# Kernel tuning notes

Hardware: AMD Instinct MI355X
Metric: run time of the kernel (lower is better)

The kernel has to match this reference:

```python
import jax, jax.numpy as jnp
import numpy as np

HEAD_SIZE = 128
B, T = 16, 2048

def setup_inputs() -> dict:
    key = jax.random.key(0)
    x = jax.random.normal(key, (B, T, 3 * HEAD_SIZE), dtype=jnp.float32)
    return {"x": x}

def reference(x) -> jnp.ndarray:
    # x: [B, T, 3*head_size] -> split into k, q, v (this order matches torch split)
    k, q, v = jnp.split(x, 3, axis=-1)  # each [B, T, D]
    d = k.shape[-1]
    scale = d ** -0.5
    # scores: [B, T, T]
    wei = jnp.einsum('bqd,bkd->bqk', q, k) * scale
    Tq = x.shape[1]
    causal = jnp.tril(jnp.ones((Tq, Tq), dtype=bool))
    wei = jnp.where(causal, wei, -jnp.inf)
    wei = jax.nn.softmax(wei, axis=-1)
    out = jnp.einsum('bqk,bkd->bqd', wei, v)  # [B, T, D]
    return out
```

## Files before the change

### kernel.cpp

```cpp
#include <hip/hip_runtime.h>

#define SEQ_T 2048
#define HDIM  128
#define NB    16
#define NTILES (SEQ_T / 64)
#define TILE_SHORTS 8192

typedef __attribute__((ext_vector_type(8))) short short8;
typedef __attribute__((ext_vector_type(4))) float float4v;
typedef __attribute__((ext_vector_type(4))) unsigned int uint4v;

#define EXP2F(x) __builtin_amdgcn_exp2f(x)

__device__ __forceinline__ unsigned int bfpack2(float a, float b) {
  unsigned int ua = __builtin_bit_cast(unsigned int, a);
  unsigned int ub = __builtin_bit_cast(unsigned int, b);
  return ((ua + 0x8000u) >> 16) | ((ub + 0x8000u) & 0xFFFF0000u);
}
__device__ __forceinline__ unsigned short f2bf(float a) {
  return (unsigned short)((__builtin_bit_cast(unsigned int, a) + 0x8000u) >> 16);
}
__device__ __forceinline__ float bf2f(unsigned short h) {
  unsigned int u = ((unsigned int)h) << 16;
  return __builtin_bit_cast(float, u);
}

__device__ __forceinline__ float dpp_max16(float x) {
  int t;
  t = __builtin_amdgcn_mov_dpp(__builtin_bit_cast(int, x), 0xB1, 0xF, 0xF, true);
  x = fmaxf(x, __builtin_bit_cast(float, t));
  t = __builtin_amdgcn_mov_dpp(__builtin_bit_cast(int, x), 0x4E, 0xF, 0xF, true);
  x = fmaxf(x, __builtin_bit_cast(float, t));
  t = __builtin_amdgcn_mov_dpp(__builtin_bit_cast(int, x), 0x141, 0xF, 0xF, true);
  x = fmaxf(x, __builtin_bit_cast(float, t));
  t = __builtin_amdgcn_mov_dpp(__builtin_bit_cast(int, x), 0x140, 0xF, 0xF, true);
  x = fmaxf(x, __builtin_bit_cast(float, t));
  return x;
}
__device__ __forceinline__ float dpp_sum16(float x) {
  int t;
  t = __builtin_amdgcn_mov_dpp(__builtin_bit_cast(int, x), 0xB1, 0xF, 0xF, true);
  x += __builtin_bit_cast(float, t);
  t = __builtin_amdgcn_mov_dpp(__builtin_bit_cast(int, x), 0x4E, 0xF, 0xF, true);
  x += __builtin_bit_cast(float, t);
  t = __builtin_amdgcn_mov_dpp(__builtin_bit_cast(int, x), 0x141, 0xF, 0xF, true);
  x += __builtin_bit_cast(float, t);
  t = __builtin_amdgcn_mov_dpp(__builtin_bit_cast(int, x), 0x140, 0xF, 0xF, true);
  x += __builtin_bit_cast(float, t);
  return x;
}

template<int CS> struct ChunkCfg;
template<> struct ChunkCfg<4> { static const int CPB = 72, SPB = 70, QB0 = 2; };
template<> struct ChunkCfg<8> { static const int CPB = 40, SPB = 36, QB0 = 4; };

__global__ __launch_bounds__(256) void prepass2(const float* __restrict__ x,
                                                unsigned short* __restrict__ kbuf,
                                                unsigned short* __restrict__ vbuf) {
  const int b = blockIdx.x >> 5;
  const int t = blockIdx.x & 31;
  const int tid = threadIdx.x;
  __shared__ __align__(16) unsigned short Klds[8192];
  __shared__ __align__(16) unsigned short Vlds[8192];

  const float* xb = x + (size_t)b * (SEQ_T * 384) + (size_t)t * 64 * 384;

  for (int i = 0; i < 8; ++i) {
    int idx = tid + i * 256;
    int row = idx >> 5, c4 = (idx & 31) << 2;
    float4v f = *(const float4v*)(xb + (size_t)row * 384 + c4);
    *(uint2*)&Klds[row * 128 + c4] = make_uint2(bfpack2(f[0], f[1]), bfpack2(f[2], f[3]));
  }
  {
    int kb = tid >> 5, db = tid & 31;
    for (int p = 0; p < 2; ++p) {
      int kbx = kb + p * 8;
      const float* vb = xb + (size_t)(4 * kbx) * 384 + 256 + 4 * db;
      float4v v0 = *(const float4v*)(vb);
      float4v v1 = *(const float4v*)(vb + 384);
      float4v v2 = *(const float4v*)(vb + 768);
      float4v v3 = *(const float4v*)(vb + 1152);
      int sl = ((kbx >> 3) << 2) | (kbx & 3);
      int o  = ((kbx >> 2) & 1) * 4;
      for (int j = 0; j < 4; ++j) {
        int d = 4 * db + j;
        *(uint2*)&Vlds[d * 64 + ((sl + d) & 7) * 8 + o] =
            make_uint2(bfpack2(v0[j], v1[j]), bfpack2(v2[j], v3[j]));
      }
    }
  }
  __syncthreads();

  unsigned short* kdst = kbuf + (size_t)blockIdx.x * TILE_SHORTS;
  unsigned short* vdst = vbuf + (size_t)blockIdx.x * TILE_SHORTS;
  for (int i = 0; i < 4; ++i) {
    int n = tid + i * 256;
    int r = n >> 4, pu = n & 15, u = (pu - r) & 15;
    *(uint4v*)&kdst[n * 8] = *(const uint4v*)&Klds[r * 128 + u * 8];
    *(uint4v*)&vdst[n * 8] = *(const uint4v*)&Vlds[n * 8];
  }
}

template<int CS>
__global__ __launch_bounds__(512, 4) void attn_chunk_k(const float* __restrict__ x,
                                                       const unsigned short* __restrict__ kbuf,
                                                       const unsigned short* __restrict__ vbuf,
                                                       unsigned short* __restrict__ Opart,
                                                       float* __restrict__ mlpart,
                                                       float* __restrict__ out) {
  const int f = blockIdx.x;
  const int b = f / ChunkCfg<CS>::CPB;
  const int c = f - b * ChunkCfg<CS>::CPB;
  int qb = 0, cum = 0;
  for (;;) {
    int gg = (2 * qb + 2 + CS - 1) / CS;
    if (c < cum + gg) break;
    cum += gg; ++qb;
  }
  const int g = (2 * qb + 2 + CS - 1) / CS;
  const int k = c - cum;
  const int sBeg = k * CS;
  const int sEnd = min(sBeg + CS, 2 * qb + 2);

  const int tid  = threadIdx.x;
  const int qt   = tid >> 6;
  const int lane = tid & 63;
  const int low  = lane & 15;
  const int quad = lane >> 4;
  const int q0   = qb * 128 + qt * 16;

  __shared__ __align__(16) unsigned char smem[32768];
  unsigned short* Ks = (unsigned short*)smem;
  unsigned short* Vt = (unsigned short*)(smem + 16384);

  const float* xb = x + (size_t)b * (SEQ_T * 3 * HDIM);
  const unsigned short* kt = kbuf + (size_t)b * NTILES * TILE_SHORTS;
  const unsigned short* vt = vbuf + (size_t)b * NTILES * TILE_SHORTS;

  const float qs = 0.08838834764831845f * 1.4426950408889634f;
  short8 qa[4];
  {
    const float* qrow = xb + (size_t)(q0 + low) * 384 + 128;
    for (int kc = 0; kc < 4; ++kc) {
      float4v f0 = *(const float4v*)(qrow + kc * 32 + quad * 8);
      float4v f1 = *(const float4v*)(qrow + kc * 32 + quad * 8 + 4);
      uint4v u = { bfpack2(f0[0] * qs, f0[1] * qs), bfpack2(f0[2] * qs, f0[3] * qs),
                   bfpack2(f1[0] * qs, f1[1] * qs), bfpack2(f1[2] * qs, f1[3] * qs) };
      qa[kc] = __builtin_bit_cast(short8, u);
    }
  }

  float4v accv[8];
  for (int i = 0; i < 8; ++i) accv[i] = (float4v){0.f, 0.f, 0.f, 0.f};
  float l = 0.f;

  const int ch = qt * 2;

  uint4v kr0, kr1, vr0, vr1;
  {
    const unsigned short* ksrc = kt + (size_t)sBeg * TILE_SHORTS;
    const unsigned short* vsrc = vt + (size_t)sBeg * TILE_SHORTS;
    kr0 = *(const uint4v*)(ksrc + (size_t)ch * 512 + lane * 8);
    kr1 = *(const uint4v*)(ksrc + (size_t)(ch + 1) * 512 + lane * 8);
    vr0 = *(const uint4v*)(vsrc + (size_t)ch * 512 + lane * 8);
    vr1 = *(const uint4v*)(vsrc + (size_t)(ch + 1) * 512 + lane * 8);
  }

  for (int s = sBeg; s < sEnd; ++s) {
    __syncthreads();

    *(uint4v*)&Ks[(size_t)ch * 512 + lane * 8]       = kr0;
    *(uint4v*)&Ks[(size_t)(ch + 1) * 512 + lane * 8] = kr1;
    *(uint4v*)&Vt[(size_t)ch * 512 + lane * 8]       = vr0;
    *(uint4v*)&Vt[(size_t)(ch + 1) * 512 + lane * 8] = vr1;

    __syncthreads();

    if (s + 1 < sEnd) {
      const unsigned short* ksrc = kt + (size_t)(s + 1) * TILE_SHORTS;
      const unsigned short* vsrc = vt + (size_t)(s + 1) * TILE_SHORTS;
      kr0 = *(const uint4v*)(ksrc + (size_t)ch * 512 + lane * 8);
      kr1 = *(const uint4v*)(ksrc + (size_t)(ch + 1) * 512 + lane * 8);
      vr0 = *(const uint4v*)(vsrc + (size_t)ch * 512 + lane * 8);
      vr1 = *(const uint4v*)(vsrc + (size_t)(ch + 1) * 512 + lane * 8);
    }

    for (int h = 0; h < 2; ++h) {
      const int c0 = s * 64 + h * 32;
      if (c0 > q0 + 15) continue;
      const int Ra = (h << 5) + low;
      const int Rb = Ra + 16;
      float4v s0 = {0.f,0.f,0.f,0.f}, s1 = {0.f,0.f,0.f,0.f};
      for (int kc = 0; kc < 4; ++kc) {
        short8 kf0 = *(const short8*)&Ks[Ra * 128 + (((kc * 4 + quad) + Ra) & 15) * 8];
        short8 kf1 = *(const short8*)&Ks[Rb * 128 + (((kc * 4 + quad) + Rb) & 15) * 8];
        s0 = __builtin_amdgcn_mfma_f32_16x16x32_bf16(kf0, qa[kc], s0, 0, 0, 0);
        s1 = __builtin_amdgcn_mfma_f32_16x16x32_bf16(kf1, qa[kc], s1, 0, 0, 0);
      }
      if (c0 + 31 > q0) {
        const int qrow = q0 + low;
        for (int r = 0; r < 4; ++r) {
          s0[r] = (c0 + quad * 4 + r      <= qrow) ? s0[r] : -1e30f;
          s1[r] = (c0 + 16 + quad * 4 + r <= qrow) ? s1[r] : -1e30f;
        }
      }
      for (int r = 0; r < 4; ++r) {
        s0[r] = EXP2F(s0[r]);
        s1[r] = EXP2F(s1[r]);
      }
      l += (s0[0] + s0[1]) + (s0[2] + s0[3]) + (s1[0] + s1[1]) + (s1[2] + s1[3]);

      uint4v pu = { bfpack2(s0[0], s0[1]), bfpack2(s0[2], s0[3]),
                    bfpack2(s1[0], s1[1]), bfpack2(s1[2], s1[3]) };
      short8 pa = __builtin_bit_cast(short8, pu);

      const int sl = (h << 2) + quad;
      for (int nt = 0; nt < 8; ++nt) {
        int d = nt * 16 + low;
        short8 vf = *(const short8*)&Vt[d * 64 + ((sl + d) & 7) * 8];
        accv[nt] = __builtin_amdgcn_mfma_f32_16x16x32_bf16(pa, vf, accv[nt], 0, 0, 0);
      }
    }
  }

  l += __shfl_xor(l, 16);
  l += __shfl_xor(l, 32);
  float lr[4];
  for (int r = 0; r < 4; ++r) lr[r] = __shfl(l, quad * 4 + r);

  if (g == 1) {
    float inv[4];
    for (int r = 0; r < 4; ++r) inv[r] = 1.f / lr[r];
    float* ob = out + ((size_t)b * SEQ_T + q0) * HDIM;
    for (int nt = 0; nt < 8; ++nt)
      for (int r = 0; r < 4; ++r)
        ob[(size_t)(quad * 4 + r) * HDIM + nt * 16 + low] = accv[nt][r] * inv[r];
  } else {
    const int slot = b * ChunkCfg<CS>::SPB + (cum - ChunkCfg<CS>::QB0) + k;
    unsigned short* op = Opart + (size_t)slot * 16384 + (size_t)qt * 16 * 128;
    for (int nt = 0; nt < 8; ++nt)
      for (int r = 0; r < 4; ++r)
        op[(size_t)(quad * 4 + r) * 128 + nt * 16 + low] = f2bf(accv[nt][r]);
    if (low == 0) {
      float* ml = mlpart + (size_t)slot * 256;
      for (int r = 0; r < 4; ++r)
        ml[qt * 16 + quad * 4 + r] = lr[r];
    }
  }
}

template<int CS>
__global__ __launch_bounds__(256) void merge_k(const unsigned short* __restrict__ Opart,
                                               const float* __restrict__ mlpart,
                                               float* __restrict__ out) {
  const int QB0 = ChunkCfg<CS>::QB0;
  const int rowsPB = (16 - QB0) * 128;
  const int ri  = blockIdx.x * 2 + (threadIdx.x >> 7);
  const int b   = ri / rowsPB;
  const int r2  = ri - b * rowsPB;
  const int qb  = QB0 + (r2 >> 7);
  const int row = r2 & 127;
  const int d   = threadIdx.x & 127;
  const int g   = (2 * qb + 2 + CS - 1) / CS;
  int cum = 0;
  for (int i = 0; i < qb; ++i) cum += (2 * i + 2 + CS - 1) / CS;
  const int s0 = b * ChunkCfg<CS>::SPB + cum - QB0;

  float num = 0.f, den = 0.f;
  for (int k = 0; k < g; ++k) {
    den += mlpart[(size_t)(s0 + k) * 256 + row];
    num += bf2f(Opart[(size_t)(s0 + k) * 16384 + (size_t)row * 128 + d]);
  }
  out[((size_t)b * SEQ_T + qb * 128 + row) * HDIM + d] = num / den;
}

__global__ __launch_bounds__(512, 4) void attn_fb(const float* __restrict__ x,
                                                  float* __restrict__ out) {
  const int b    = blockIdx.y;
  const int qblk = (int)gridDim.x - 1 - (int)blockIdx.x;
  const int qb0  = qblk << 6;
  const int tid  = threadIdx.x;
  const int wave = tid >> 6;
  const int lane = tid & 63;
  const int low  = lane & 15;
  const int quad = lane >> 4;
  const int qt   = wave & 3;
  const int half = wave >> 2;
  const int q0   = qb0 + (qt << 4);
  __shared__ __align__(16) unsigned char smem[48128];
  unsigned short* Ks = (unsigned short*)smem;
  unsigned short* Vt = (unsigned short*)(smem + 17408);
  unsigned short* Ps = (unsigned short*)(smem + 37888);
  float* Om = (float*)smem;
  float* Ml = (float*)(smem + 33792);
  const float* xb = x + (size_t)b * (SEQ_T * 3 * HDIM);
  const float qs = 0.08838834764831845f * 1.4426950408889634f;
  short8 qa[4];
  {
    const float* qrow = xb + (size_t)(q0 + low) * 384 + 128;
    for (int kc = 0; kc < 4; ++kc) {
      float4v f0 = *(const float4v*)(qrow + kc * 32 + quad * 8);
      float4v f1 = *(const float4v*)(qrow + kc * 32 + quad * 8 + 4);
      uint4v u = { bfpack2(f0[0] * qs, f0[1] * qs), bfpack2(f0[2] * qs, f0[3] * qs),
                   bfpack2(f1[0] * qs, f1[1] * qs), bfpack2(f1[2] * qs, f1[3] * qs) };
      qa[kc] = __builtin_bit_cast(short8, u);
    }
  }
  float4v accv[8];
  for (int i = 0; i < 8; ++i) accv[i] = (float4v){0.f, 0.f, 0.f, 0.f};
  float m_i[4] = {-1e30f, -1e30f, -1e30f, -1e30f};
  float l_i[4] = {0.f, 0.f, 0.f, 0.f};
  const int nsuper = qblk + 1;
  for (int s = 0; s < nsuper; ++s) {
    const int r0 = s << 6;
    __syncthreads();
    for (int i = 0; i < 4; ++i) {
      int f = tid + (i << 9);
      int row = f >> 5;
      int c4 = (f & 31) << 2;
      float4v kf = *(const float4v*)(xb + (size_t)(r0 + row) * 384 + c4);
      *(uint2*)&Ks[(row >> 5) * 4352 + (row & 31) * 136 + c4] =
          make_uint2(bfpack2(kf[0], kf[1]), bfpack2(kf[2], kf[3]));
    }
    {
      int kb = tid >> 5, db = tid & 31;
      int til = kb >> 3, kbl = kb & 7;
      const float* vbase = xb + (size_t)(r0 + 4 * kb) * 384 + 256 + 4 * db;
      float4v v0 = *(const float4v*)(vbase);
      float4v v1 = *(const float4v*)(vbase + 384);
      float4v v2 = *(const float4v*)(vbase + 768);
      float4v v3 = *(const float4v*)(vbase + 1152);
      unsigned short* vv = Vt + til * 5120;
      for (int j = 0; j < 4; ++j) {
        int d = 4 * db + j;
        int pb = ((kbl >> 1) + (d >> 3)) & 3;
        *(uint2*)&vv[d * 40 + pb * 8 + (kbl & 1) * 4] =
            make_uint2(bfpack2(v0[j], v1[j]), bfpack2(v2[j], v3[j]));
      }
    }
    __syncthreads();
    const int c0 = r0 + (half << 5);
    if (c0 <= q0 + 15) {
      const unsigned short* Ksp = Ks + half * 4352;
      const unsigned short* Vtp = Vt + half * 5120;
      float4v s0 = {0.f,0.f,0.f,0.f}, s1 = {0.f,0.f,0.f,0.f};
      for (int kc = 0; kc < 4; ++kc) {
        short8 kf0 = *(const short8*)&Ksp[low * 136 + kc * 32 + quad * 8];
        short8 kf1 = *(const short8*)&Ksp[(16 + low) * 136 + kc * 32 + quad * 8];
        s0 = __builtin_amdgcn_mfma_f32_16x16x32_bf16(qa[kc], kf0, s0, 0, 0, 0);
        s1 = __builtin_amdgcn_mfma_f32_16x16x32_bf16(qa[kc], kf1, s1, 0, 0, 0);
      }
      if (c0 + 31 > q0) {
        for (int r = 0; r < 4; ++r) {
          int qrow = q0 + quad * 4 + r;
          s0[r] = (c0 + low      <= qrow) ? s0[r] : -1e30f;
          s1[r] = (c0 + 16 + low <= qrow) ? s1[r] : -1e30f;
        }
      }
      float rmax[4], alpha[4];
      for (int r = 0; r < 4; ++r) rmax[r] = dpp_max16(fmaxf(s0[r], s1[r]));
      for (int r = 0; r < 4; ++r) {
        float mn = fmaxf(m_i[r], rmax[r]);
        alpha[r] = EXP2F(m_i[r] - mn);
        m_i[r] = mn;
      }
      for (int r = 0; r < 4; ++r) {
        s0[r] = EXP2F(s0[r] - m_i[r]);
        s1[r] = EXP2F(s1[r] - m_i[r]);
      }
      float rs[4];
      for (int r = 0; r < 4; ++r) rs[r] = dpp_sum16(s0[r] + s1[r]);
      for (int r = 0; r < 4; ++r) l_i[r] = l_i[r] * alpha[r] + rs[r];
      for (int nt = 0; nt < 8; ++nt)
        for (int r = 0; r < 4; ++r) accv[nt][r] *= alpha[r];
      unsigned short* pw = Ps + wave * 640;
      for (int r = 0; r < 4; ++r) {
        int row = quad * 4 + r;
        pw[row * 40 + low]      = f2bf(s0[r]);
        pw[row * 40 + 16 + low] = f2bf(s1[r]);
      }
      short8 pa = *(const short8*)&pw[low * 40 + quad * 8];
      for (int nt = 0; nt < 8; ++nt) {
        int d = nt * 16 + low;
        int pb = (quad + (d >> 3)) & 3;
        short8 vf = *(const short8*)&Vtp[d * 40 + pb * 8];
        accv[nt] = __builtin_amdgcn_mfma_f32_16x16x32_bf16(pa, vf, accv[nt], 0, 0, 0);
      }
    }
  }
  __syncthreads();
  if (half == 1) {
    float* om = Om + qt * 2112;
    for (int nt = 0; nt < 8; ++nt)
      for (int r = 0; r < 4; ++r)
        om[(quad * 4 + r) * 132 + nt * 16 + low] = accv[nt][r];
    if (low == 0) {
      for (int r = 0; r < 4; ++r) {
        Ml[qt * 32 + quad * 4 + r]      = m_i[r];
        Ml[qt * 32 + 16 + quad * 4 + r] = l_i[r];
      }
    }
  }
  __syncthreads();
  if (half == 0) {
    float aA[4], aB[4], linv[4];
    for (int r = 0; r < 4; ++r) {
      float mB = Ml[qt * 32 + quad * 4 + r];
      float lB = Ml[qt * 32 + 16 + quad * 4 + r];
      float mN = fmaxf(m_i[r], mB);
      aA[r] = EXP2F(m_i[r] - mN);
      aB[r] = EXP2F(mB - mN);
      linv[r] = 1.f / (l_i[r] * aA[r] + lB * aB[r]);
    }
    const float* om = Om + qt * 2112;
    float* ob = out + ((size_t)b * SEQ_T + q0) * HDIM;
    for (int nt = 0; nt < 8; ++nt)
      for (int r = 0; r < 4; ++r) {
        float o = accv[nt][r] * aA[r] + om[(quad * 4 + r) * 132 + nt * 16 + low] * aB[r];
        ob[(size_t)(quad * 4 + r) * HDIM + nt * 16 + low] = o * linv[r];
      }
  }
}

extern "C" void kernel_launch(void* const* d_in, const int* in_sizes, int n_in,
                              void* d_out, int out_size, void* d_ws, size_t ws_size,
                              hipStream_t stream) {
  const float* x = (const float*)d_in[0];
  float* out = (float*)d_out;
  const size_t PRE = (size_t)NB * NTILES * TILE_SHORTS * 2 * sizeof(unsigned short);

  const size_t OP4 = (size_t)NB * 70 * 16384 * sizeof(unsigned short);
  const size_t ML4 = (size_t)NB * 70 * 256 * sizeof(float);
  const size_t OP8 = (size_t)NB * 36 * 16384 * sizeof(unsigned short);
  const size_t ML8 = (size_t)NB * 36 * 256 * sizeof(float);

  unsigned short* kbuf = (unsigned short*)d_ws;
  unsigned short* vbuf = kbuf + (size_t)NB * NTILES * TILE_SHORTS;

  if (ws_size >= PRE + OP4 + ML4) {
    unsigned short* Opart = (unsigned short*)((char*)d_ws + PRE);
    float*          mlp   = (float*)((char*)d_ws + PRE + OP4);
    hipLaunchKernelGGL(prepass2, dim3(NB * NTILES), dim3(256), 0, stream, x, kbuf, vbuf);
    hipLaunchKernelGGL((attn_chunk_k<4>), dim3(NB * 72), dim3(512), 0, stream,
                       x, kbuf, vbuf, Opart, mlp, out);
    hipLaunchKernelGGL((merge_k<4>), dim3(NB * 14 * 128 / 2), dim3(256), 0, stream,
                       Opart, mlp, out);
  } else if (ws_size >= PRE + OP8 + ML8) {
    unsigned short* Opart = (unsigned short*)((char*)d_ws + PRE);
    float*          mlp   = (float*)((char*)d_ws + PRE + OP8);
    hipLaunchKernelGGL(prepass2, dim3(NB * NTILES), dim3(256), 0, stream, x, kbuf, vbuf);
    hipLaunchKernelGGL((attn_chunk_k<8>), dim3(NB * 40), dim3(512), 0, stream,
                       x, kbuf, vbuf, Opart, mlp, out);
    hipLaunchKernelGGL((merge_k<8>), dim3(NB * 12 * 128 / 2), dim3(256), 0, stream,
                       Opart, mlp, out);
  } else {
    hipLaunchKernelGGL(attn_fb, dim3(SEQ_T / 64, NB), dim3(512), 0, stream, x, out);
  }
}
```

Baseline: 141.0 us.

## Double-buffer K/V LDS in 32-key half tiles with one barrier per step

```diff
diff --git a/kernel.cpp b/kernel.cpp
--- a/kernel.cpp
+++ b/kernel.cpp
@@ -80,11 +80,12 @@
       float4v v1 = *(const float4v*)(vb + 384);
       float4v v2 = *(const float4v*)(vb + 768);
       float4v v3 = *(const float4v*)(vb + 1152);
-      int sl = ((kbx >> 3) << 2) | (kbx & 3);
+      int hh = kbx >> 3;
+      int sl = kbx & 3;
       int o  = ((kbx >> 2) & 1) * 4;
       for (int j = 0; j < 4; ++j) {
         int d = 4 * db + j;
-        *(uint2*)&Vlds[d * 64 + ((sl + d) & 7) * 8 + o] =
+        *(uint2*)&Vlds[hh * 4096 + d * 32 + ((sl + d) & 3) * 8 + o] =
             make_uint2(bfpack2(v0[j], v1[j]), bfpack2(v2[j], v3[j]));
       }
     }
@@ -129,9 +130,7 @@
   const int quad = lane >> 4;
   const int q0   = qb * 128 + qt * 16;
 
-  __shared__ __align__(16) unsigned char smem[32768];
-  unsigned short* Ks = (unsigned short*)smem;
-  unsigned short* Vt = (unsigned short*)(smem + 16384);
+  __shared__ __align__(16) unsigned short smem[16384];
 
   const float* xb = x + (size_t)b * (SEQ_T * 3 * HDIM);
   const unsigned short* kt = kbuf + (size_t)b * NTILES * TILE_SHORTS;
@@ -154,42 +153,43 @@
   for (int i = 0; i < 8; ++i) accv[i] = (float4v){0.f, 0.f, 0.f, 0.f};
   float l = 0.f;
 
-  const int ch = qt * 2;
-
-  uint4v kr0, kr1, vr0, vr1;
+  const int so = qt * 512 + lane * 8;
+
+  const int tBeg = 2 * sBeg, tEnd = 2 * sEnd;
+#define HTOFF(t) ((size_t)((t) >> 1) * TILE_SHORTS + (size_t)(((t) & 1)) * 4096 + so)
+
+  uint4v kr, vr;
   {
-    const unsigned short* ksrc = kt + (size_t)sBeg * TILE_SHORTS;
-    const unsigned short* vsrc = vt + (size_t)sBeg * TILE_SHORTS;
-    kr0 = *(const uint4v*)(ksrc + (size_t)ch * 512 + lane * 8);
-    kr1 = *(const uint4v*)(ksrc + (size_t)(ch + 1) * 512 + lane * 8);
-    vr0 = *(const uint4v*)(vsrc + (size_t)ch * 512 + lane * 8);
-    vr1 = *(const uint4v*)(vsrc + (size_t)(ch + 1) * 512 + lane * 8);
-  }
-
-  for (int s = sBeg; s < sEnd; ++s) {
+    uint4v k0 = *(const uint4v*)(kt + HTOFF(tBeg));
+    uint4v v0 = *(const uint4v*)(vt + HTOFF(tBeg));
+    *(uint4v*)&smem[so]        = k0;
+    *(uint4v*)&smem[4096 + so] = v0;
+  }
+  if (tBeg + 1 < tEnd) {
+    kr = *(const uint4v*)(kt + HTOFF(tBeg + 1));
+    vr = *(const uint4v*)(vt + HTOFF(tBeg + 1));
+  }
+
+  int cur = 0;
+  for (int t = tBeg; t < tEnd; ++t) {
     __syncthreads();
 
-    *(uint4v*)&Ks[(size_t)ch * 512 + lane * 8]       = kr0;
-    *(uint4v*)&Ks[(size_t)(ch + 1) * 512 + lane * 8] = kr1;
-    *(uint4v*)&Vt[(size_t)ch * 512 + lane * 8]       = vr0;
-    *(uint4v*)&Vt[(size_t)(ch + 1) * 512 + lane * 8] = vr1;
-
-    __syncthreads();
-
-    if (s + 1 < sEnd) {
-      const unsigned short* ksrc = kt + (size_t)(s + 1) * TILE_SHORTS;
-      const unsigned short* vsrc = vt + (size_t)(s + 1) * TILE_SHORTS;
-      kr0 = *(const uint4v*)(ksrc + (size_t)ch * 512 + lane * 8);
-      kr1 = *(const uint4v*)(ksrc + (size_t)(ch + 1) * 512 + lane * 8);
-      vr0 = *(const uint4v*)(vsrc + (size_t)ch * 512 + lane * 8);
-      vr1 = *(const uint4v*)(vsrc + (size_t)(ch + 1) * 512 + lane * 8);
-    }
-
-    for (int h = 0; h < 2; ++h) {
-      const int c0 = s * 64 + h * 32;
-      if (c0 > q0 + 15) continue;
-      const int Ra = (h << 5) + low;
-      const int Rb = Ra + 16;
+    if (t + 1 < tEnd) {
+      unsigned short* Kb = smem + (cur ^ 1) * 8192;
+      *(uint4v*)&Kb[so]        = kr;
+      *(uint4v*)&Kb[4096 + so] = vr;
+    }
+    if (t + 2 < tEnd) {
+      kr = *(const uint4v*)(kt + HTOFF(t + 2));
+      vr = *(const uint4v*)(vt + HTOFF(t + 2));
+    }
+
+    const int c0 = t * 32;
+    if (c0 <= q0 + 15) {
+      const unsigned short* Ks = smem + cur * 8192;
+      const unsigned short* Vh = Ks + 4096;
+      const int Ra = low;
+      const int Rb = low + 16;
       float4v s0 = {0.f,0.f,0.f,0.f}, s1 = {0.f,0.f,0.f,0.f};
       for (int kc = 0; kc < 4; ++kc) {
         short8 kf0 = *(const short8*)&Ks[Ra * 128 + (((kc * 4 + quad) + Ra) & 15) * 8];
@@ -214,14 +214,15 @@
                     bfpack2(s1[0], s1[1]), bfpack2(s1[2], s1[3]) };
       short8 pa = __builtin_bit_cast(short8, pu);
 
-      const int sl = (h << 2) + quad;
       for (int nt = 0; nt < 8; ++nt) {
         int d = nt * 16 + low;
-        short8 vf = *(const short8*)&Vt[d * 64 + ((sl + d) & 7) * 8];
+        short8 vf = *(const short8*)&Vh[d * 32 + ((quad + d) & 3) * 8];
         accv[nt] = __builtin_amdgcn_mfma_f32_16x16x32_bf16(pa, vf, accv[nt], 0, 0, 0);
       }
     }
-  }
+    cur ^= 1;
+  }
+#undef HTOFF
 
   l += __shfl_xor(l, 16);
   l += __shfl_xor(l, 32);
```

Measured after the change: 143.9 us. 2.0% more time.
